# Optimization experiments

Measured on AMD Instinct MI355X. Metric: run time of the kernel, lower is better.

Reference implementation:

```python
import jax, jax.numpy as jnp
import numpy as np

BSZ = 2048
L = 64            # sequence length, power of 2
D = 15            # symbol_repr_size
NC = 10           # n_classes; embedding row NC is the 'inf' token
TREE_LEN = 2 * L - 1  # next_power_of_2(L)*2 - 1


def rms_norm(x):
    # x / (sqrt(mean(x^2, -1) + 1e-6) + 1e-6)
    return x / (jnp.sqrt(jnp.mean(x * x, axis=-1, keepdims=True) + 1e-6) + 1e-6)


def setup_inputs() -> dict:
    key = jax.random.key(0)
    k1, k2, k3, k4, k5 = jax.random.split(key, 5)
    x = jax.random.randint(k1, (BSZ, L), 0, NC)
    q = jnp.sort(jax.random.randint(k2, (BSZ, 2), 0, L), axis=1)  # low <= high
    query_low, query_high = q[:, 0], q[:, 1]
    emb = jax.random.normal(k3, (NC + 1, D), dtype=jnp.float32)
    W_lin = jax.random.normal(k4, (NC, D), dtype=jnp.float32) * 0.26   # ~1/sqrt(D)
    W_rule = jax.random.normal(k5, (2, D * D), dtype=jnp.float32) * 0.066  # ~1/D
    return {"emb": emb, "W_lin": W_lin, "W_rule": W_rule,
            "x": x, "query_low": query_low, "query_high": query_high}


def reference(emb, W_lin, W_rule, x, query_low, query_high):
    def combine(a, b):
        # outer product [b, D, D] -> rule linear (225 -> 2) -> softmax mix
        inp = jnp.einsum('bi,bj->bij', a, b).reshape(a.shape[0], -1)
        alpha = jax.nn.softmax(inp @ W_rule.T, axis=-1)  # [b, 2]
        return alpha[:, :1] * a + alpha[:, 1:] * b

    def build(trees, lst, low, high, pos):
        # recursive segment-tree build; low/high/pos are static Python ints
        if low == high:
            return rms_norm(trees.at[:, pos, :].set(lst[:, low, :]))
        mid = (low + high) // 2
        trees = build(trees, lst, low, mid, 2 * pos + 1)
        trees = build(trees, lst, mid + 1, high, 2 * pos + 2)
        mix = combine(trees[:, 2 * pos + 1], trees[:, 2 * pos + 2])
        return rms_norm(trees.at[:, pos, :].set(mix))

    inf_raw = emb[NC]  # raw inf token used inside query (no rms_norm in torch)

    def query(trees, returns, low, high, pos):
        if pos >= TREE_LEN:
            return returns
        f = returns.dtype
        mA = ((query_low <= low) & (query_high >= high)).astype(f)[:, None]
        returns = mA * trees[:, pos] + (1 - mA) * returns
        mB = ((query_low > high) | (query_high < low)).astype(f)[:, None]
        returns = mB * inf_raw[None, :] + (1 - mB) * returns
        mC = (1 - mA) * (1 - mB)
        mid = (low + high) // 2
        a1 = query(trees, returns, low, mid, 2 * pos + 1)
        a2 = query(trees, returns, mid + 1, high, 2 * pos + 2)
        new = combine(a1, a2)
        return rms_norm(mC * new + (1 - mC) * returns)

    h = rms_norm(emb[x])                              # [BSZ, L, D]
    inf_n = rms_norm(emb[NC][None, None, :])          # normalized inf token
    trees = jnp.broadcast_to(inf_n, (BSZ, TREE_LEN, D)) + jnp.zeros((), emb.dtype)
    trees = build(trees, h, 0, L - 1, 0)              # [BSZ, TREE_LEN, D]
    returns = jnp.zeros((BSZ, D), dtype=emb.dtype)
    returns = query(trees, returns, 0, L - 1, 0)      # [BSZ, D]
    return returns @ W_lin.T                          # [BSZ, NC]
```

## Files before the change

kernel.cpp:

```cpp
#include <hip/hip_runtime.h>
#include <math.h>

#define DD 15
#define DP 20
#define LL 64
#define NCC 10
#define NTREE 63
#define EPB 4

__device__ __forceinline__ float dpp_xor1(float x) {
    return __int_as_float(__builtin_amdgcn_update_dpp(0, __float_as_int(x), 0xB1, 0xF, 0xF, true));
}
__device__ __forceinline__ float dpp_xor2(float x) {
    return __int_as_float(__builtin_amdgcn_update_dpp(0, __float_as_int(x), 0x4E, 0xF, 0xF, true));
}
__device__ __forceinline__ float dpp_hmirror(float x) {
    return __int_as_float(__builtin_amdgcn_update_dpp(0, __float_as_int(x), 0x141, 0xF, 0xF, true));
}

struct CR {
    float4 Lq;
    float4 R0, R1, R2, R3;
    float2 lm, rm;
};

__device__ __forceinline__ CR load_children(const float* Lrow, const float* Rrow, int qr, int u) {
    CR c;
    c.Lq = ((const float4*)Lrow)[qr];
    c.R0 = ((const float4*)Rrow)[0];
    c.R1 = ((const float4*)Rrow)[1];
    c.R2 = ((const float4*)Rrow)[2];
    c.R3 = ((const float4*)Rrow)[3];
    c.lm = ((const float2*)Lrow)[u];
    c.rm = ((const float2*)Rrow)[u];
    return c;
}

__device__ __forceinline__ void compute_combine(const CR& c, const float w[4][DD], int k,
                                                float& o0, float& o1)
{
    float Bv[DD] = {c.R0.x,c.R0.y,c.R0.z,c.R0.w, c.R1.x,c.R1.y,c.R1.z,c.R1.w,
                    c.R2.x,c.R2.y,c.R2.z,c.R2.w, c.R3.x,c.R3.y,c.R3.z};
    float Av[4] = {c.Lq.x, c.Lq.y, c.Lq.z, c.Lq.w};

    float p = 0.f;
    #pragma unroll
    for (int ri = 0; ri < 4; ++ri) {
        float dA = 0.f, dB = 0.f;
        #pragma unroll
        for (int j = 0; j < 8; ++j)  dA = fmaf(w[ri][j], Bv[j], dA);
        #pragma unroll
        for (int j = 8; j < DD; ++j) dB = fmaf(w[ri][j], Bv[j], dB);
        p = fmaf(Av[ri], dA + dB, p);
    }
    float a    = p + dpp_xor2(p);
    float hma  = dpp_hmirror(a);
    float self = a + dpp_xor1(hma);
    float oth  = dpp_xor1(a) + hma;
    float aS = __builtin_amdgcn_rcpf(1.0f + __expf(oth - self));
    float aO = 1.0f - aS;
    float a0 = (k == 0) ? aS : aO;
    float a1 = (k == 0) ? aO : aS;

    float v0 = fmaf(a0, c.lm.x, a1 * c.rm.x);
    float v1 = fmaf(a0, c.lm.y, a1 * c.rm.y);
    float ss = v0 * v0 + v1 * v1;
    ss += dpp_xor1(ss);
    ss += dpp_xor2(ss);
    ss += dpp_hmirror(ss);
    float inv = __builtin_amdgcn_rsqf(ss * (1.0f / DD) + 1e-6f);
    o0 = v0 * inv; o1 = v1 * inv;
}

template<int LVL>
__device__ __forceinline__ void phase(float (*tw)[DP], const float (*nemb)[DP],
                                      const float w[4][DD], int t, int k, int qr, int u, int g,
                                      int ql, int qh)
{
    constexpr int n = 1 << LVL, first = n - 1;
    constexpr int NB = (n > 8) ? (n / 8) : 1;
    constexpr int sh = 6 - LVL, shc = sh - 1;

    CR cb[NB]; int pb[NB];
    #pragma unroll
    for (int st = 0; st < NB; ++st) {
        int pi = (n >= 8) ? (st * 8 + g) : (g & (n - 1));
        int p = first + pi;
        pb[st] = p;
        cb[st] = load_children(&tw[2 * p + 1][0], &tw[2 * p + 2][0], qr, u);
    }
    const int g2 = (t >> 3) & 1;
    int bnd = g2 ? qh : ql;
    int piq = bnd >> sh;
    int pq = first + piq;
    int lo = piq << sh, hi = lo + (1 << sh) - 1;
    bool full = (ql <= lo) && (qh >= hi);
    int lo1 = (2 * piq) << shc,     hi1 = lo1 + (1 << shc) - 1;
    int lo2 = (2 * piq + 1) << shc, hi2 = lo2 + (1 << shc) - 1;
    bool d1 = (ql > hi1) || (qh < lo1);
    bool d2 = (ql > hi2) || (qh < lo2);
    const float* Lp = d1 ? &nemb[NCC][0] : &tw[2 * pq + 1][0];
    const float* Rp = d2 ? &nemb[NCC][0] : &tw[2 * pq + 2][0];
    CR cq = load_children(Lp, Rp, qr, u);

    #pragma unroll
    for (int st = 0; st < NB; ++st) {
        float o0, o1;
        compute_combine(cb[st], w, k, o0, o1);
        if (n >= 8 || g < n)
            ((float2*)&tw[pb[st]][0])[u] = make_float2(o0, o1);
    }
    {
        float o0, o1;
        compute_combine(cq, w, k, o0, o1);
        bool we = (!full) && (t < 16) && (g2 == 0 || piq != (ql >> sh));
        if (we) ((float2*)&tw[pq][0])[u] = make_float2(o0, o1);
    }
}

extern "C" __global__ __attribute__((amdgpu_flat_work_group_size(256, 256)))
void seg_tree_kernel(
    const float* __restrict__ emb,
    const float* __restrict__ W_lin,
    const float* __restrict__ W_rule,
    const int*  __restrict__ x,
    const int*  __restrict__ qlo_g,
    const int*  __restrict__ qhi_g,
    float* __restrict__ out,
    int bsz)
{
    __shared__ __align__(16) float nemb[NCC + 1][DP];
    __shared__ __align__(16) float tree[EPB][NTREE][DP];

    const int tb = threadIdx.x;
    const int wv = tb >> 6;
    const int t  = tb & 63;
    int b = blockIdx.x * EPB + wv;
    const bool active = (b < bsz);
    if (!active) b = bsz - 1;

    const int k = t & 1, qr = (t >> 1) & 3, u = t & 7, g = t >> 3;
    float (*tw)[DP] = tree[wv];

    const int ql = qlo_g[b], qh = qhi_g[b];

    int xA[4], xB[4];
    #pragma unroll
    for (int st = 0; st < 4; ++st) {
        xA[st] = x[b * LL + st * 16 + 2 * g];
        xB[st] = x[b * LL + st * 16 + 2 * g + 1];
    }
    const int g2i = (t >> 3) & 1;
    int piB = (g2i ? qh : ql) >> 1;
    int xq1 = x[b * LL + 2 * piB], xq2 = x[b * LL + 2 * piB + 1];

    float w[4][DD];
    #pragma unroll
    for (int ri = 0; ri < 4; ++ri) {
        int i = 4 * qr + ri;
        bool valid = (i < DD);
        const float* src = W_rule + k * DD * DD + (valid ? i * DD : 0);
        #pragma unroll
        for (int j = 0; j < DD; ++j) w[ri][j] = valid ? src[j] : 0.0f;
    }
    #pragma unroll
    for (int ri = 0; ri < 4; ++ri)
        #pragma unroll
        for (int j = 0; j < DD; ++j)
            asm("" : "+v"(w[ri][j]));

    float wl[DD];
    {
        const float* wlp = W_lin + ((t < NCC) ? t : 0) * DD;
        #pragma unroll
        for (int d = 0; d < DD; ++d) wl[d] = wlp[d];
    }

    if (tb < NCC + 1) {
        float v[DD]; float ssum = 0.f;
        #pragma unroll
        for (int d = 0; d < DD; ++d) { v[d] = emb[tb * DD + d]; ssum += v[d] * v[d]; }
        float inv = __builtin_amdgcn_rsqf(ssum * (1.0f / DD) + 1e-6f);
        #pragma unroll
        for (int d = 0; d < DD; ++d) nemb[tb][d] = v[d] * inv;
        nemb[tb][DD] = 0.0f;
    }
    __syncthreads();

    {
        CR c5[4];
        #pragma unroll
        for (int st = 0; st < 4; ++st)
            c5[st] = load_children(&nemb[xA[st]][0], &nemb[xB[st]][0], qr, u);
        int lo = 2 * piB, hi = lo + 1;
        bool full5 = (ql <= lo) && (qh >= hi);
        bool d1 = (ql > lo) || (qh < lo);
        bool d2 = (ql > hi) || (qh < hi);
        const float* Lp = d1 ? &nemb[NCC][0] : &nemb[xq1][0];
        const float* Rp = d2 ? &nemb[NCC][0] : &nemb[xq2][0];
        CR cq5 = load_children(Lp, Rp, qr, u);

        #pragma unroll
        for (int st = 0; st < 4; ++st) {
            float o0, o1;
            compute_combine(c5[st], w, k, o0, o1);
            ((float2*)&tw[31 + st * 8 + g][0])[u] = make_float2(o0, o1);
        }
        {
            float o0, o1;
            compute_combine(cq5, w, k, o0, o1);
            bool we = (!full5) && (t < 16) && (g2i == 0 || piB != (ql >> 1));
            if (we) ((float2*)&tw[31 + piB][0])[u] = make_float2(o0, o1);
        }
    }

    phase<4>(tw, nemb, w, t, k, qr, u, g, ql, qh);
    phase<3>(tw, nemb, w, t, k, qr, u, g, ql, qh);
    phase<2>(tw, nemb, w, t, k, qr, u, g, ql, qh);
    phase<1>(tw, nemb, w, t, k, qr, u, g, ql, qh);

    {
        bool d1 = (ql > 31);
        bool d2 = (qh < 32);
        const float* Lp = d1 ? &nemb[NCC][0] : &tw[1][0];
        const float* Rp = d2 ? &nemb[NCC][0] : &tw[2][0];
        CR c0 = load_children(Lp, Rp, qr, u);
        float o0, o1;
        compute_combine(c0, w, k, o0, o1);
        if (t < 8) ((float2*)&tw[0][0])[u] = make_float2(o0, o1);
    }

    if (active && t < NCC) {
        float acc = 0.f;
        #pragma unroll
        for (int d = 0; d < DD; ++d) acc = fmaf(tw[0][d], wl[d], acc);
        out[b * NCC + t] = acc;
    }
}

extern "C" void kernel_launch(void* const* d_in, const int* in_sizes, int n_in,
                              void* d_out, int out_size, void* d_ws, size_t ws_size,
                              hipStream_t stream) {
    const float* emb    = (const float*)d_in[0];
    const float* W_lin  = (const float*)d_in[1];
    const float* W_rule = (const float*)d_in[2];
    const int*   x      = (const int*)d_in[3];
    const int*   qlo    = (const int*)d_in[4];
    const int*   qhi    = (const int*)d_in[5];
    float* outp = (float*)d_out;

    int bsz = in_sizes[3] / LL;
    int nblk = (bsz + EPB - 1) / EPB;
    seg_tree_kernel<<<dim3(nblk), dim3(256), 0, stream>>>(
        emb, W_lin, W_rule, x, qlo, qhi, outp, bsz);
}
```

Baseline: 15.50 us.

## Replace unrolled per-level phases with rolled loop over full-length tree

Stages the normalized leaf embeddings into a 127-entry shared tree and runs all six levels in one non-unrolled loop, replacing the templated, fully unrolled phases that batched child loads into registers. The goal is smaller code and lower register pressure, so more waves fit and instruction-cache misses drop. The cost is losing the load batching that overlapped LDS latency with compute, plus loop overhead and more LDS use per block. Query bounds are also made wave-uniform with readfirstlane.

```diff
diff --git a/kernel.cpp b/kernel.cpp
--- a/kernel.cpp
+++ b/kernel.cpp
@@ -5,7 +5,7 @@
 #define DP 20
 #define LL 64
 #define NCC 10
-#define NTREE 63
+#define TL 127
 #define EPB 4
 
 __device__ __forceinline__ float dpp_xor1(float x) {
@@ -18,30 +18,20 @@
     return __int_as_float(__builtin_amdgcn_update_dpp(0, __float_as_int(x), 0x141, 0xF, 0xF, true));
 }
 
-struct CR {
-    float4 Lq;
-    float4 R0, R1, R2, R3;
-    float2 lm, rm;
-};
-
-__device__ __forceinline__ CR load_children(const float* Lrow, const float* Rrow, int qr, int u) {
-    CR c;
-    c.Lq = ((const float4*)Lrow)[qr];
-    c.R0 = ((const float4*)Rrow)[0];
-    c.R1 = ((const float4*)Rrow)[1];
-    c.R2 = ((const float4*)Rrow)[2];
-    c.R3 = ((const float4*)Rrow)[3];
-    c.lm = ((const float2*)Lrow)[u];
-    c.rm = ((const float2*)Rrow)[u];
-    return c;
-}
-
-__device__ __forceinline__ void compute_combine(const CR& c, const float w[4][DD], int k,
-                                                float& o0, float& o1)
+__device__ __forceinline__ void combine_ptr(const float* Lrow, const float* Rrow,
+                                            const float w[4][DD], int k, int qr, int u,
+                                            float& o0, float& o1)
 {
-    float Bv[DD] = {c.R0.x,c.R0.y,c.R0.z,c.R0.w, c.R1.x,c.R1.y,c.R1.z,c.R1.w,
-                    c.R2.x,c.R2.y,c.R2.z,c.R2.w, c.R3.x,c.R3.y,c.R3.z};
-    float Av[4] = {c.Lq.x, c.Lq.y, c.Lq.z, c.Lq.w};
+    float4 R0 = ((const float4*)Rrow)[0];
+    float4 R1 = ((const float4*)Rrow)[1];
+    float4 R2 = ((const float4*)Rrow)[2];
+    float4 R3 = ((const float4*)Rrow)[3];
+    float4 Aq = ((const float4*)Lrow)[qr];
+    float2 lm = ((const float2*)Lrow)[u];
+    float2 rm = ((const float2*)Rrow)[u];
+    float Bv[DD] = {R0.x,R0.y,R0.z,R0.w, R1.x,R1.y,R1.z,R1.w,
+                    R2.x,R2.y,R2.z,R2.w, R3.x,R3.y,R3.z};
+    float Av[4] = {Aq.x, Aq.y, Aq.z, Aq.w};
 
     float p = 0.f;
     #pragma unroll
@@ -62,60 +52,14 @@
     float a0 = (k == 0) ? aS : aO;
     float a1 = (k == 0) ? aO : aS;
 
-    float v0 = fmaf(a0, c.lm.x, a1 * c.rm.x);
-    float v1 = fmaf(a0, c.lm.y, a1 * c.rm.y);
+    float v0 = fmaf(a0, lm.x, a1 * rm.x);
+    float v1 = fmaf(a0, lm.y, a1 * rm.y);
     float ss = v0 * v0 + v1 * v1;
     ss += dpp_xor1(ss);
     ss += dpp_xor2(ss);
     ss += dpp_hmirror(ss);
     float inv = __builtin_amdgcn_rsqf(ss * (1.0f / DD) + 1e-6f);
     o0 = v0 * inv; o1 = v1 * inv;
-}
-
-template<int LVL>
-__device__ __forceinline__ void phase(float (*tw)[DP], const float (*nemb)[DP],
-                                      const float w[4][DD], int t, int k, int qr, int u, int g,
-                                      int ql, int qh)
-{
-    constexpr int n = 1 << LVL, first = n - 1;
-    constexpr int NB = (n > 8) ? (n / 8) : 1;
-    constexpr int sh = 6 - LVL, shc = sh - 1;
-
-    CR cb[NB]; int pb[NB];
-    #pragma unroll
-    for (int st = 0; st < NB; ++st) {
-        int pi = (n >= 8) ? (st * 8 + g) : (g & (n - 1));
-        int p = first + pi;
-        pb[st] = p;
-        cb[st] = load_children(&tw[2 * p + 1][0], &tw[2 * p + 2][0], qr, u);
-    }
-    const int g2 = (t >> 3) & 1;
-    int bnd = g2 ? qh : ql;
-    int piq = bnd >> sh;
-    int pq = first + piq;
-    int lo = piq << sh, hi = lo + (1 << sh) - 1;
-    bool full = (ql <= lo) && (qh >= hi);
-    int lo1 = (2 * piq) << shc,     hi1 = lo1 + (1 << shc) - 1;
-    int lo2 = (2 * piq + 1) << shc, hi2 = lo2 + (1 << shc) - 1;
-    bool d1 = (ql > hi1) || (qh < lo1);
-    bool d2 = (ql > hi2) || (qh < lo2);
-    const float* Lp = d1 ? &nemb[NCC][0] : &tw[2 * pq + 1][0];
-    const float* Rp = d2 ? &nemb[NCC][0] : &tw[2 * pq + 2][0];
-    CR cq = load_children(Lp, Rp, qr, u);
-
-    #pragma unroll
-    for (int st = 0; st < NB; ++st) {
-        float o0, o1;
-        compute_combine(cb[st], w, k, o0, o1);
-        if (n >= 8 || g < n)
-            ((float2*)&tw[pb[st]][0])[u] = make_float2(o0, o1);
-    }
-    {
-        float o0, o1;
-        compute_combine(cq, w, k, o0, o1);
-        bool we = (!full) && (t < 16) && (g2 == 0 || piq != (ql >> sh));
-        if (we) ((float2*)&tw[pq][0])[u] = make_float2(o0, o1);
-    }
 }
 
 extern "C" __global__ __attribute__((amdgpu_flat_work_group_size(256, 256)))
@@ -130,7 +74,7 @@
     int bsz)
 {
     __shared__ __align__(16) float nemb[NCC + 1][DP];
-    __shared__ __align__(16) float tree[EPB][NTREE][DP];
+    __shared__ __align__(16) float tree[EPB][TL][DP];
 
     const int tb = threadIdx.x;
     const int wv = tb >> 6;
@@ -140,19 +84,13 @@
     if (!active) b = bsz - 1;
 
     const int k = t & 1, qr = (t >> 1) & 3, u = t & 7, g = t >> 3;
+    const int g2 = (t >> 3) & 1;
     float (*tw)[DP] = tree[wv];
 
-    const int ql = qlo_g[b], qh = qhi_g[b];
+    const int ql = __builtin_amdgcn_readfirstlane(qlo_g[b]);
+    const int qh = __builtin_amdgcn_readfirstlane(qhi_g[b]);
 
-    int xA[4], xB[4];
-    #pragma unroll
-    for (int st = 0; st < 4; ++st) {
-        xA[st] = x[b * LL + st * 16 + 2 * g];
-        xB[st] = x[b * LL + st * 16 + 2 * g + 1];
-    }
-    const int g2i = (t >> 3) & 1;
-    int piB = (g2i ? qh : ql) >> 1;
-    int xq1 = x[b * LL + 2 * piB], xq2 = x[b * LL + 2 * piB + 1];
+    const int xi = x[b * LL + t];
 
     float w[4][DD];
     #pragma unroll
@@ -187,47 +125,45 @@
     }
     __syncthreads();
 
-    {
-        CR c5[4];
-        #pragma unroll
-        for (int st = 0; st < 4; ++st)
-            c5[st] = load_children(&nemb[xA[st]][0], &nemb[xB[st]][0], qr, u);
-        int lo = 2 * piB, hi = lo + 1;
-        bool full5 = (ql <= lo) && (qh >= hi);
-        bool d1 = (ql > lo) || (qh < lo);
-        bool d2 = (ql > hi) || (qh < hi);
-        const float* Lp = d1 ? &nemb[NCC][0] : &nemb[xq1][0];
-        const float* Rp = d2 ? &nemb[NCC][0] : &nemb[xq2][0];
-        CR cq5 = load_children(Lp, Rp, qr, u);
+    #pragma unroll
+    for (int j = 0; j < 4; ++j)
+        ((float4*)&tw[63 + t][0])[j] = ((const float4*)&nemb[xi][0])[j];
 
-        #pragma unroll
-        for (int st = 0; st < 4; ++st) {
-            float o0, o1;
-            compute_combine(c5[st], w, k, o0, o1);
-            ((float2*)&tw[31 + st * 8 + g][0])[u] = make_float2(o0, o1);
+    #pragma clang loop unroll(disable)
+    for (int lvl = 5; lvl >= 0; --lvl) {
+        const int n = 1 << lvl, first = n - 1;
+        const int sh = 6 - lvl, shc = sh - 1;
+
+        if (lvl > 0) {
+            const int nst = (n > 8) ? (n >> 3) : 1;
+            #pragma clang loop unroll(disable)
+            for (int st = 0; st < nst; ++st) {
+                int pi = (n >= 8) ? (st * 8 + g) : (g & (n - 1));
+                int p = first + pi;
+                float o0, o1;
+                combine_ptr(&tw[2 * p + 1][0], &tw[2 * p + 2][0], w, k, qr, u, o0, o1);
+                if (n >= 8 || g < n)
+                    ((float2*)&tw[p][0])[u] = make_float2(o0, o1);
+            }
         }
         {
+            int bnd = g2 ? qh : ql;
+            int piq = bnd >> sh;
+            int p = first + piq;
+            int lo = piq << sh, hi = lo + (1 << sh) - 1;
+            bool full = (ql <= lo) && (qh >= hi);
+            int lo1 = (2 * piq) << shc,     hi1 = lo1 + (1 << shc) - 1;
+            int lo2 = (2 * piq + 1) << shc, hi2 = lo2 + (1 << shc) - 1;
+            bool d1 = (ql > hi1) || (qh < lo1);
+            bool d2 = (ql > hi2) || (qh < lo2);
+            const float* Lp = d1 ? &nemb[NCC][0] : &tw[2 * p + 1][0];
+            const float* Rp = d2 ? &nemb[NCC][0] : &tw[2 * p + 2][0];
             float o0, o1;
-            compute_combine(cq5, w, k, o0, o1);
-            bool we = (!full5) && (t < 16) && (g2i == 0 || piB != (ql >> 1));
-            if (we) ((float2*)&tw[31 + piB][0])[u] = make_float2(o0, o1);
+            combine_ptr(Lp, Rp, w, k, qr, u, o0, o1);
+            bool we = (t < 16) && (lvl == 0 ? (g2 == 0)
+                                            : (!full && (g2 == 0 || piq != (ql >> sh))));
+            if (we) ((float2*)&tw[p][0])[u] = make_float2(o0, o1);
         }
-    }
-
-    phase<4>(tw, nemb, w, t, k, qr, u, g, ql, qh);
-    phase<3>(tw, nemb, w, t, k, qr, u, g, ql, qh);
-    phase<2>(tw, nemb, w, t, k, qr, u, g, ql, qh);
-    phase<1>(tw, nemb, w, t, k, qr, u, g, ql, qh);
-
-    {
-        bool d1 = (ql > 31);
-        bool d2 = (qh < 32);
-        const float* Lp = d1 ? &nemb[NCC][0] : &tw[1][0];
-        const float* Rp = d2 ? &nemb[NCC][0] : &tw[2][0];
-        CR c0 = load_children(Lp, Rp, qr, u);
-        float o0, o1;
-        compute_combine(c0, w, k, o0, o1);
-        if (t < 8) ((float2*)&tw[0][0])[u] = make_float2(o0, o1);
     }
 
     if (active && t < NCC) {
```

After: 16.99 us. 1.1x slower.
